# Optimization experiments

Hardware: AMD Instinct MI355X
Metric: run time of the kernel (lower is better)

The kernel has to match this reference:

```python
import jax, jax.numpy as jnp
import numpy as np

B, IN_CAPS, IN_DIMS = 64, 2048, 8
N_CAPS, DIMS = 32, 16
R_ITER = 3
EPSILON = 1e-7  # tf.keras.backend.epsilon()
SOFTPLUS_C = float(np.log(np.expm1(1.0)))  # tfp IndependentNormal scale shift


def setup_inputs() -> dict:
    key = jax.random.key(0)
    k1, k2, k3, k4 = jax.random.split(key, 4)
    flat = IN_CAPS * N_CAPS * DIMS * IN_DIMS
    return {
        "x": jax.random.normal(k1, (B, IN_CAPS, IN_DIMS), dtype=jnp.float32),
        "loc": jax.random.normal(k2, (flat,), dtype=jnp.float32) * 0.05,
        "scale_raw": jax.random.normal(k3, (flat,), dtype=jnp.float32) * 0.1,
        "eps": jax.random.normal(k4, (flat,), dtype=jnp.float32),
    }


def squash(v, axis=-1):
    s2 = jnp.sum(jnp.square(v), axis=axis, keepdims=True)
    return (s2 / (1.0 + s2)) * v / jnp.sqrt(s2 + EPSILON)


def reference(x, loc, scale_raw, eps):
    # Bayesian posterior sample: W = loc + scale * eps (tfp IndependentNormal)
    scale = 1e-5 + jax.nn.softplus(SOFTPLUS_C + scale_raw)
    W = (loc + scale * eps).reshape(IN_CAPS, N_CAPS, DIMS, IN_DIMS)
    # predictions u_hat[b,i,j,d] = sum_k W[i,j,d,k] * x[b,i,k]
    u_hat = jnp.einsum('ijdk,bik->bijd', W, x)
    # dynamic routing
    b_logits = jnp.zeros((x.shape[0], IN_CAPS, N_CAPS), dtype=x.dtype)
    for i in range(R_ITER):
        c = jax.nn.softmax(b_logits, axis=2)          # routing weights over output caps
        s = jnp.einsum('bij,bijd->bjd', c, u_hat)     # weighted sum over input caps
        v = squash(s, axis=-1)                        # [B, N_CAPS, DIMS]
        if i < R_ITER - 1:
            b_logits = b_logits + jnp.einsum('bijd,bjd->bij', u_hat, v)
    routing_weights = c[..., None, None]              # [B, IN_CAPS, N_CAPS, 1, 1]
    return v, routing_weights
```

## Files before the change

kernel.cpp:

```cpp
#include <hip/hip_runtime.h>
#include <math.h>

#define N_B 64
#define N_ICAPS 2048
#define N_IDIMS 8
#define N_NCAPS 32
#define N_DIMS 16

__device__ __forceinline__ float softplus_f(float z) {
    return (z > 15.0f) ? z : log1pf(__expf(z));
}

__global__ __launch_bounds__(256) void compute_w(const float4* __restrict__ loc,
                                                 const float4* __restrict__ sr,
                                                 const float4* __restrict__ eps,
                                                 float4* __restrict__ W) {
    const float C = 0.5413248546129181f;
    int idx = blockIdx.x * 256 + threadIdx.x;
    float4 l = loc[idx], s = sr[idx], e = eps[idx];
    float4 o;
    o.x = fmaf(1e-5f + softplus_f(C + s.x), e.x, l.x);
    o.y = fmaf(1e-5f + softplus_f(C + s.y), e.y, l.y);
    o.z = fmaf(1e-5f + softplus_f(C + s.z), e.z, l.z);
    o.w = fmaf(1e-5f + softplus_f(C + s.w), e.w, l.w);
    W[idx] = o;
}

template<int T>
__global__ __launch_bounds__(512, 2) void route_pass(
        const float* __restrict__ W, const float* __restrict__ x,
        const float* __restrict__ v0, const float* __restrict__ v1,
        float* __restrict__ s_part, float* __restrict__ c_out) {
    __shared__ float s_lds[4 * 512];
    const int tid = threadIdx.x;
    const int w = tid >> 6;
    const int l = tid & 63;
    const int B = blockIdx.x;
    const int xcd = B & 7;
    const int q = B >> 3;
    const int ci = xcd * 8 + (q & 7);
    const int bg = q >> 3;
    const int b0 = bg * 4;
    const int i0 = ci * 32 + w * 4;
    const int j = l >> 1;
    const int d0 = (l & 1) * 8;

    float sacc[4][8];
    #pragma unroll
    for (int a = 0; a < 4; ++a)
        #pragma unroll
        for (int c2 = 0; c2 < 8; ++c2) sacc[a][c2] = 0.0f;

    for (int ii = 0; ii < 4; ++ii) {
        const int i = i0 + ii;
        float Wr[64];
        const float4* wp = reinterpret_cast<const float4*>(W + (size_t)i * 4096 + l * 64);
        #pragma unroll
        for (int qq = 0; qq < 16; ++qq) {
            float4 t = wp[qq];
            Wr[qq * 4 + 0] = t.x; Wr[qq * 4 + 1] = t.y;
            Wr[qq * 4 + 2] = t.z; Wr[qq * 4 + 3] = t.w;
        }
        #pragma unroll
        for (int bb = 0; bb < 4; ++bb) {
            const int b = b0 + bb;
            const float4* xp = reinterpret_cast<const float4*>(x + ((size_t)b * N_ICAPS + i) * N_IDIMS);
            float4 xa = xp[0], xb = xp[1];
            float xr[8] = {xa.x, xa.y, xa.z, xa.w, xb.x, xb.y, xb.z, xb.w};
            float u[8];
            #pragma unroll
            for (int dd = 0; dd < 8; ++dd) {
                float acc = 0.0f;
                #pragma unroll
                for (int k = 0; k < 8; ++k) acc = fmaf(Wr[dd * 8 + k], xr[k], acc);
                u[dd] = acc;
            }
            float c;
            if (T == 0) {
                c = 1.0f / 32.0f;
            } else {
                float lg = 0.0f;
                {
                    const float4* vp = reinterpret_cast<const float4*>(v0 + ((size_t)b * N_NCAPS + j) * N_DIMS + d0);
                    float4 va = vp[0], vb = vp[1];
                    float vr[8] = {va.x, va.y, va.z, va.w, vb.x, vb.y, vb.z, vb.w};
                    #pragma unroll
                    for (int dd = 0; dd < 8; ++dd) lg = fmaf(u[dd], vr[dd], lg);
                }
                if (T == 2) {
                    const float4* vp = reinterpret_cast<const float4*>(v1 + ((size_t)b * N_NCAPS + j) * N_DIMS + d0);
                    float4 va = vp[0], vb = vp[1];
                    float vr[8] = {va.x, va.y, va.z, va.w, vb.x, vb.y, vb.z, vb.w};
                    #pragma unroll
                    for (int dd = 0; dd < 8; ++dd) lg = fmaf(u[dd], vr[dd], lg);
                }
                lg += __shfl_xor(lg, 1);
                float m = lg;
                #pragma unroll
                for (int mask = 2; mask < 64; mask <<= 1) m = fmaxf(m, __shfl_xor(m, mask));
                float e = __expf(lg - m);
                float ssum = e;
                #pragma unroll
                for (int mask = 2; mask < 64; mask <<= 1) ssum += __shfl_xor(ssum, mask);
                c = e / ssum;
                if (T == 2 && d0 == 0)
                    c_out[((size_t)b * N_ICAPS + i) * N_NCAPS + j] = c;
            }
            #pragma unroll
            for (int dd = 0; dd < 8; ++dd) sacc[bb][dd] = fmaf(c, u[dd], sacc[bb][dd]);
        }
    }

    for (int idx = tid; idx < 2048; idx += 512) s_lds[idx] = 0.0f;
    __syncthreads();
    #pragma unroll
    for (int bb = 0; bb < 4; ++bb)
        #pragma unroll
        for (int dd = 0; dd < 8; ++dd) {
            atomicAdd(&s_lds[bb * 512 + l * 8 + dd], sacc[bb][dd]);
        }
    __syncthreads();
    for (int idx = tid; idx < 2048; idx += 512) {
        int bb = idx >> 9, jd = idx & 511;
        s_part[((size_t)ci * 64 + b0 + bb) * 512 + jd] = s_lds[idx];
    }
}

__global__ __launch_bounds__(512) void reduce_squash(const float* __restrict__ s_part,
                                                     float* __restrict__ v_out) {
    const int b = blockIdx.x;
    const int tid = threadIdx.x;
    float acc = 0.0f;
    #pragma unroll 8
    for (int ci = 0; ci < 64; ++ci) acc += s_part[((size_t)ci * 64 + b) * 512 + tid];
    float s2 = acc * acc;
    #pragma unroll
    for (int mask = 1; mask < 16; mask <<= 1) s2 += __shfl_xor(s2, mask);
    float vv = acc * (s2 / (1.0f + s2)) * (1.0f / sqrtf(s2 + 1e-7f));
    v_out[(size_t)b * 512 + tid] = vv;
}

extern "C" void kernel_launch(void* const* d_in, const int* in_sizes, int n_in,
                              void* d_out, int out_size, void* d_ws, size_t ws_size,
                              hipStream_t stream) {
    const float* x   = (const float*)d_in[0];
    const float* loc = (const float*)d_in[1];
    const float* sr  = (const float*)d_in[2];
    const float* eps = (const float*)d_in[3];
    float* out = (float*)d_out;

    float* W      = (float*)d_ws;
    float* s_part = W + 8388608;
    float* v0b    = s_part + 2097152;
    float* v1b    = v0b + 32768;
    float* c_out  = out + 32768;

    compute_w<<<8192, 256, 0, stream>>>((const float4*)loc, (const float4*)sr,
                                        (const float4*)eps, (float4*)W);
    route_pass<0><<<1024, 512, 0, stream>>>(W, x, nullptr, nullptr, s_part, nullptr);
    reduce_squash<<<64, 512, 0, stream>>>(s_part, v0b);
    route_pass<1><<<1024, 512, 0, stream>>>(W, x, v0b, nullptr, s_part, nullptr);
    reduce_squash<<<64, 512, 0, stream>>>(s_part, v1b);
    route_pass<2><<<1024, 512, 0, stream>>>(W, x, v0b, v1b, s_part, c_out);
    reduce_squash<<<64, 512, 0, stream>>>(s_part, out);
}
```

Before: 653.7 us.

## Transpose W layout for coalesced loads and batch softmax shuffles across batch rows

compute_w now writes W in an interleaved layout so each lane's float4 loads in route_pass are strided by 64 float4s, which makes wavefront accesses contiguous (coalesced). The routing pass splits the per-batch loop into a logits phase and an accumulate phase. This lets the softmax shuffle reductions for four batch rows interleave and drops the max-subtraction step. It recomputes u in the second phase instead of keeping it in registers, and the exp without max subtraction risks overflow if the logits grow large.

```diff
diff --git a/kernel.cpp b/kernel.cpp
--- a/kernel.cpp
+++ b/kernel.cpp
@@ -14,16 +14,22 @@
 __global__ __launch_bounds__(256) void compute_w(const float4* __restrict__ loc,
                                                  const float4* __restrict__ sr,
                                                  const float4* __restrict__ eps,
-                                                 float4* __restrict__ W) {
+                                                 float4* __restrict__ W2) {
     const float C = 0.5413248546129181f;
-    int idx = blockIdx.x * 256 + threadIdx.x;
-    float4 l = loc[idx], s = sr[idx], e = eps[idx];
+    int f = blockIdx.x * 256 + threadIdx.x;
+    float4 l = loc[f], s = sr[f], e = eps[f];
     float4 o;
     o.x = fmaf(1e-5f + softplus_f(C + s.x), e.x, l.x);
     o.y = fmaf(1e-5f + softplus_f(C + s.y), e.y, l.y);
     o.z = fmaf(1e-5f + softplus_f(C + s.z), e.z, l.z);
     o.w = fmaf(1e-5f + softplus_f(C + s.w), e.w, l.w);
-    W[idx] = o;
+    int i    = f >> 10;
+    int j    = (f >> 5) & 31;
+    int d    = (f >> 1) & 15;
+    int kh   = f & 1;
+    int lcol = j * 2 + (d >> 3);
+    int qq   = (d & 7) * 2 + kh;
+    W2[((size_t)i << 10) + qq * 64 + lcol] = o;
 }
 
 template<int T>
@@ -54,31 +60,45 @@
     for (int ii = 0; ii < 4; ++ii) {
         const int i = i0 + ii;
         float Wr[64];
-        const float4* wp = reinterpret_cast<const float4*>(W + (size_t)i * 4096 + l * 64);
+        const float4* wp = reinterpret_cast<const float4*>(W) + ((size_t)i << 10) + l;
         #pragma unroll
         for (int qq = 0; qq < 16; ++qq) {
-            float4 t = wp[qq];
+            float4 t = wp[qq * 64];
             Wr[qq * 4 + 0] = t.x; Wr[qq * 4 + 1] = t.y;
             Wr[qq * 4 + 2] = t.z; Wr[qq * 4 + 3] = t.w;
         }
-        #pragma unroll
-        for (int bb = 0; bb < 4; ++bb) {
-            const int b = b0 + bb;
-            const float4* xp = reinterpret_cast<const float4*>(x + ((size_t)b * N_ICAPS + i) * N_IDIMS);
-            float4 xa = xp[0], xb = xp[1];
-            float xr[8] = {xa.x, xa.y, xa.z, xa.w, xb.x, xb.y, xb.z, xb.w};
-            float u[8];
-            #pragma unroll
-            for (int dd = 0; dd < 8; ++dd) {
-                float acc = 0.0f;
-                #pragma unroll
-                for (int k = 0; k < 8; ++k) acc = fmaf(Wr[dd * 8 + k], xr[k], acc);
-                u[dd] = acc;
-            }
-            float c;
-            if (T == 0) {
-                c = 1.0f / 32.0f;
-            } else {
+
+        if (T == 0) {
+            #pragma unroll
+            for (int bb = 0; bb < 4; ++bb) {
+                const int b = b0 + bb;
+                const float4* xp = reinterpret_cast<const float4*>(x + ((size_t)b * N_ICAPS + i) * N_IDIMS);
+                float4 xa = xp[0], xb = xp[1];
+                float xr[8] = {xa.x, xa.y, xa.z, xa.w, xb.x, xb.y, xb.z, xb.w};
+                #pragma unroll
+                for (int dd = 0; dd < 8; ++dd) {
+                    float acc = 0.0f;
+                    #pragma unroll
+                    for (int k = 0; k < 8; ++k) acc = fmaf(Wr[dd * 8 + k], xr[k], acc);
+                    sacc[bb][dd] = fmaf(0.03125f, acc, sacc[bb][dd]);
+                }
+            }
+        } else {
+            float lgh[4];
+            #pragma unroll
+            for (int bb = 0; bb < 4; ++bb) {
+                const int b = b0 + bb;
+                const float4* xp = reinterpret_cast<const float4*>(x + ((size_t)b * N_ICAPS + i) * N_IDIMS);
+                float4 xa = xp[0], xb = xp[1];
+                float xr[8] = {xa.x, xa.y, xa.z, xa.w, xb.x, xb.y, xb.z, xb.w};
+                float u[8];
+                #pragma unroll
+                for (int dd = 0; dd < 8; ++dd) {
+                    float acc = 0.0f;
+                    #pragma unroll
+                    for (int k = 0; k < 8; ++k) acc = fmaf(Wr[dd * 8 + k], xr[k], acc);
+                    u[dd] = acc;
+                }
                 float lg = 0.0f;
                 {
                     const float4* vp = reinterpret_cast<const float4*>(v0 + ((size_t)b * N_NCAPS + j) * N_DIMS + d0);
@@ -94,20 +114,41 @@
                     #pragma unroll
                     for (int dd = 0; dd < 8; ++dd) lg = fmaf(u[dd], vr[dd], lg);
                 }
-                lg += __shfl_xor(lg, 1);
-                float m = lg;
-                #pragma unroll
-                for (int mask = 2; mask < 64; mask <<= 1) m = fmaxf(m, __shfl_xor(m, mask));
-                float e = __expf(lg - m);
-                float ssum = e;
-                #pragma unroll
-                for (int mask = 2; mask < 64; mask <<= 1) ssum += __shfl_xor(ssum, mask);
-                c = e / ssum;
-                if (T == 2 && d0 == 0)
-                    c_out[((size_t)b * N_ICAPS + i) * N_NCAPS + j] = c;
-            }
-            #pragma unroll
-            for (int dd = 0; dd < 8; ++dd) sacc[bb][dd] = fmaf(c, u[dd], sacc[bb][dd]);
+                lgh[bb] = lg;
+            }
+            float ef[4], ss[4], cr[4];
+            #pragma unroll
+            for (int bb = 0; bb < 4; ++bb) lgh[bb] += __shfl_xor(lgh[bb], 1);
+            #pragma unroll
+            for (int bb = 0; bb < 4; ++bb) ef[bb] = __expf(lgh[bb]);
+            #pragma unroll
+            for (int bb = 0; bb < 4; ++bb) ss[bb] = ef[bb];
+            #pragma unroll
+            for (int mask = 2; mask < 64; mask <<= 1)
+                #pragma unroll
+                for (int bb = 0; bb < 4; ++bb) ss[bb] += __shfl_xor(ss[bb], mask);
+            #pragma unroll
+            for (int bb = 0; bb < 4; ++bb)
+                cr[bb] = ef[bb] / ss[bb];
+            if (T == 2 && d0 == 0) {
+                #pragma unroll
+                for (int bb = 0; bb < 4; ++bb)
+                    c_out[(((size_t)(b0 + bb)) * N_ICAPS + i) * N_NCAPS + j] = cr[bb];
+            }
+            #pragma unroll
+            for (int bb = 0; bb < 4; ++bb) {
+                const int b = b0 + bb;
+                const float4* xp = reinterpret_cast<const float4*>(x + ((size_t)b * N_ICAPS + i) * N_IDIMS);
+                float4 xa = xp[0], xb = xp[1];
+                float xr[8] = {xa.x, xa.y, xa.z, xa.w, xb.x, xb.y, xb.z, xb.w};
+                #pragma unroll
+                for (int dd = 0; dd < 8; ++dd) {
+                    float acc = 0.0f;
+                    #pragma unroll
+                    for (int k = 0; k < 8; ++k) acc = fmaf(Wr[dd * 8 + k], xr[k], acc);
+                    sacc[bb][dd] = fmaf(cr[bb], acc, sacc[bb][dd]);
+                }
+            }
         }
     }
 
```

Measured after the change: 524.7 us. 19.7% less time.
